# Kernel tuning notes

Hardware: AMD Instinct MI355X
Metric: run time of the kernel (lower is better)

## Reference

```python
import jax, jax.numpy as jnp
import numpy as np

E, C, D, F = 8, 2048, 2048, 8192  # experts, capacity/expert, d_model, d_ff


def setup_inputs() -> dict:
    key = jax.random.key(0)
    k_in, k_w1, k_w2 = jax.random.split(key, 3)
    inputs = jax.random.normal(k_in, (1, E * C, D), dtype=jnp.float32)
    w1 = jax.random.normal(k_w1, (E, D, F), dtype=jnp.float32) * (D ** -0.5)
    b1 = jnp.zeros((E, F), dtype=jnp.float32)
    w2 = jax.random.normal(k_w2, (E, F, D), dtype=jnp.float32) * (F ** -0.5)
    b2 = jnp.zeros((E, D), dtype=jnp.float32)
    return {"inputs": inputs, "w1": w1, "b1": b1, "w2": w2, "b2": b2}


def reference(inputs, w1, b1, w2, b2):
    # inputs: [B, E*C, D]; chunk(dim=1) into E equal chunks == reshape to [B, E, C, D]
    e = w1.shape[0]
    b_, t, d = inputs.shape
    x = inputs.reshape(b_, e, t // e, d)                       # [B,E,C,D]
    # Per-expert FFN: Linear(D->F) + GELU + Linear(F->D), batched over experts
    h = jax.nn.gelu(jnp.einsum("becd,edf->becf", x, w1) + b1[None, :, None, :])
    out = jnp.einsum("becf,efd->becd", h, w2) + b2[None, :, None, :]
    # concat over experts on dim=1 == reshape back to [B, E*C, D]
    return out.reshape(b_, t, d)
```

## Files before the change

### kernel.cpp

```cpp
#include <hip/hip_runtime.h>
#include <hip/hip_bf16.h>
#include <stdint.h>

#define E_ 8
#define C_ 2048
#define D_ 2048
#define F_ 8192

typedef __bf16 bf16x8 __attribute__((ext_vector_type(8)));
typedef float floatx4 __attribute__((ext_vector_type(4)));
typedef uint32_t uint32x4 __attribute__((ext_vector_type(4)));

__device__ __forceinline__ uint16_t f2bf_rne(float f) {
    uint32_t u = __builtin_bit_cast(uint32_t, f);
    u += 0x7fffu + ((u >> 16) & 1u);
    return (uint16_t)(u >> 16);
}

__device__ __forceinline__ float gelu_tanh(float x) {
    float z = 0.7978845608028654f * x * (1.0f + 0.044715f * x * x);
    float e = __expf(2.0f * z);
    float t = 1.0f - 2.0f / (e + 1.0f);
    return 0.5f * x * (1.0f + t);
}

__global__ __launch_bounds__(256) void convert_x_kernel(const float* __restrict__ in,
                                                        uint16_t* __restrict__ out, int n8) {
    int i = blockIdx.x * 256 + threadIdx.x;
    if (i >= n8) return;
    const floatx4* pin = (const floatx4*)in;
    floatx4 a = pin[2 * i];
    floatx4 b = pin[2 * i + 1];
    uint32x4 w;
    w[0] = (uint32_t)f2bf_rne(a[0]) | ((uint32_t)f2bf_rne(a[1]) << 16);
    w[1] = (uint32_t)f2bf_rne(a[2]) | ((uint32_t)f2bf_rne(a[3]) << 16);
    w[2] = (uint32_t)f2bf_rne(b[0]) | ((uint32_t)f2bf_rne(b[1]) << 16);
    w[3] = (uint32_t)f2bf_rne(b[2]) | ((uint32_t)f2bf_rne(b[3]) << 16);
    ((uint32x4*)out)[i] = w;
}

__global__ __launch_bounds__(256) void transpose_convert_kernel(
    const float* __restrict__ in, uint16_t* __restrict__ out,
    int K, int N, int tiles_k, int tiles_n) {
    __shared__ float lds[64 * 65];
    int tiles = tiles_k * tiles_n;
    int e = blockIdx.x / tiles;
    int t = blockIdx.x % tiles;
    int tk = t % tiles_k;
    int tn = t / tiles_k;
    size_t ebase = (size_t)e * K * N;
    int k0 = tk * 64, n0 = tn * 64;
    const float* ip = in + ebase + (size_t)k0 * N + n0;
    int tid = threadIdx.x;
#pragma unroll
    for (int i = 0; i < 4; i++) {
        int lin = i * 256 + tid;
        int r = lin >> 4, c = lin & 15;
        floatx4 v = *(const floatx4*)(ip + (size_t)r * N + c * 4);
        float* l = &lds[r * 65 + c * 4];
        l[0] = v[0]; l[1] = v[1]; l[2] = v[2]; l[3] = v[3];
    }
    __syncthreads();
    uint16_t* op = out + ebase + (size_t)n0 * K + k0;
#pragma unroll
    for (int i = 0; i < 2; i++) {
        int lin = i * 256 + tid;
        int n = lin >> 3, c = lin & 7;
        uint32x4 w;
#pragma unroll
        for (int j = 0; j < 4; j++) {
            float f0 = lds[(c * 8 + 2 * j) * 65 + n];
            float f1 = lds[(c * 8 + 2 * j + 1) * 65 + n];
            w[j] = (uint32_t)f2bf_rne(f0) | ((uint32_t)f2bf_rne(f1) << 16);
        }
        *(uint32x4*)(op + (size_t)n * K + c * 8) = w;
    }
}

template <int GELU>
__global__ __launch_bounds__(256) void gemm_bt_kernel(
    const uint16_t* __restrict__ A,
    const uint16_t* __restrict__ Bt,
    const float* __restrict__ bias,
    void* __restrict__ Out,
    int M, int N, int K, int tiles_m, int tiles_n) {
    __shared__ uint16_t As[128 * 64];
    __shared__ uint16_t Bs[128 * 64];
    int tiles = tiles_m * tiles_n;
    int e = blockIdx.x / tiles;
    int t = blockIdx.x % tiles;
    int bm = t % tiles_m;
    int bn = t / tiles_m;
    int tid = threadIdx.x;
    int lane = tid & 63;
    int wid = tid >> 6;
    int wm = wid >> 1, wn = wid & 1;

    const uint16_t* Ae = A + (size_t)e * M * K;
    const uint16_t* Be = Bt + (size_t)e * N * K;

    int srow = lane >> 3;
    int skk = (lane & 7) * 8;
    const uint16_t* ag[4];
    const uint16_t* bg[4];
#pragma unroll
    for (int j = 0; j < 4; j++) {
        int ch = wid * 4 + j;
        ag[j] = Ae + (size_t)(bm * 128 + ch * 8 + srow) * K + skk;
        bg[j] = Be + (size_t)(bn * 128 + ch * 8 + srow) * K + skk;
    }

    floatx4 acc[4][4];
#pragma unroll
    for (int i = 0; i < 4; i++)
#pragma unroll
        for (int j = 0; j < 4; j++)
#pragma unroll
            for (int r = 0; r < 4; r++) acc[i][j][r] = 0.0f;

    int aoff[4], boff[4];
#pragma unroll
    for (int i = 0; i < 4; i++) {
        aoff[i] = (wm * 64 + i * 16 + (lane & 15)) * 64 + (lane >> 4) * 8;
        boff[i] = (wn * 64 + i * 16 + (lane & 15)) * 64 + (lane >> 4) * 8;
    }

    int kt = K >> 6;
    for (int k0 = 0; k0 < kt; k0++) {
#pragma unroll
        for (int j = 0; j < 4; j++) {
            __builtin_amdgcn_global_load_lds(
                (const __attribute__((address_space(1))) uint32_t*)ag[j],
                (__attribute__((address_space(3))) uint32_t*)&As[(wid * 4 + j) * 512], 16, 0, 0);
            __builtin_amdgcn_global_load_lds(
                (const __attribute__((address_space(1))) uint32_t*)bg[j],
                (__attribute__((address_space(3))) uint32_t*)&Bs[(wid * 4 + j) * 512], 16, 0, 0);
            ag[j] += 64;
            bg[j] += 64;
        }
        __syncthreads();
#pragma unroll
        for (int ks = 0; ks < 2; ks++) {
            bf16x8 fa[4], fb[4];
#pragma unroll
            for (int i = 0; i < 4; i++) {
                fa[i] = *(const bf16x8*)&As[aoff[i] + ks * 32];
                fb[i] = *(const bf16x8*)&Bs[boff[i] + ks * 32];
            }
#pragma unroll
            for (int i = 0; i < 4; i++)
#pragma unroll
                for (int j = 0; j < 4; j++)
                    acc[i][j] = __builtin_amdgcn_mfma_f32_16x16x32_bf16(fa[i], fb[j], acc[i][j], 0, 0, 0);
        }
        __syncthreads();
    }

    int col0 = bn * 128 + wn * 64 + (lane & 15);
    int row0 = bm * 128 + wm * 64 + (lane >> 4) * 4;
    const float* be = bias + (size_t)e * N;
    if (GELU) {
        uint16_t* O = (uint16_t*)Out + (size_t)e * M * N;
#pragma unroll
        for (int j = 0; j < 4; j++) {
            int col = col0 + j * 16;
            float bv = be[col];
#pragma unroll
            for (int i = 0; i < 4; i++) {
                int row = row0 + i * 16;
#pragma unroll
                for (int r = 0; r < 4; r++) {
                    float v = acc[i][j][r] + bv;
                    O[(size_t)(row + r) * N + col] = f2bf_rne(gelu_tanh(v));
                }
            }
        }
    } else {
        float* O = (float*)Out + (size_t)e * M * N;
#pragma unroll
        for (int j = 0; j < 4; j++) {
            int col = col0 + j * 16;
            float bv = be[col];
#pragma unroll
            for (int i = 0; i < 4; i++) {
                int row = row0 + i * 16;
#pragma unroll
                for (int r = 0; r < 4; r++) {
                    O[(size_t)(row + r) * N + col] = acc[i][j][r] + bv;
                }
            }
        }
    }
}

extern "C" void kernel_launch(void* const* d_in, const int* in_sizes, int n_in,
                              void* d_out, int out_size, void* d_ws, size_t ws_size,
                              hipStream_t stream) {
    (void)in_sizes; (void)n_in; (void)out_size; (void)ws_size;
    const float* x  = (const float*)d_in[0];
    const float* w1 = (const float*)d_in[1];
    const float* b1 = (const float*)d_in[2];
    const float* w2 = (const float*)d_in[3];
    const float* b2 = (const float*)d_in[4];
    float* out = (float*)d_out;

    uint16_t* Xb = (uint16_t*)d_ws;
    uint16_t* Wt = Xb + (size_t)E_ * C_ * D_;
    uint16_t* Hb = Wt + (size_t)E_ * D_ * F_;

    int n8 = (E_ * C_ * D_) / 8;
    convert_x_kernel<<<n8 / 256, 256, 0, stream>>>(x, Xb, n8);

    transpose_convert_kernel<<<E_ * (D_ / 64) * (F_ / 64), 256, 0, stream>>>(
        w1, Wt, D_, F_, D_ / 64, F_ / 64);

    gemm_bt_kernel<1><<<E_ * (C_ / 128) * (F_ / 128), 256, 0, stream>>>(
        Xb, Wt, b1, Hb, C_, F_, D_, C_ / 128, F_ / 128);

    transpose_convert_kernel<<<E_ * (F_ / 64) * (D_ / 64), 256, 0, stream>>>(
        w2, Wt, F_, D_, F_ / 64, D_ / 64);

    gemm_bt_kernel<0><<<E_ * (C_ / 128) * (D_ / 128), 256, 0, stream>>>(
        Hb, Wt, b2, out, C_, D_, F_, C_ / 128, D_ / 128);
}
```

Baseline: 2.929 ms.

## Triple-buffer GEMM K-loop with async global-to-LDS prefetch two stages ahead

Restructures the bf16 GEMM main loop into a three-buffer LDS pipeline with a K-step of 32. Loads for step k+2 are issued before the MFMAs of step k, and each step uses a single barrier with explicit vmcnt/lgkmcnt waits. This hides global-memory latency behind compute and removes one barrier per iteration. It also sets launch bounds for 3 blocks per CU and raises wave priority around the MFMA block. The trade-off is more LDS per block, smaller K-steps (more barriers per unit of work) and hand-written wait counts that must match the number of outstanding loads exactly.

```diff
diff --git a/kernel.cpp b/kernel.cpp
--- a/kernel.cpp
+++ b/kernel.cpp
@@ -77,15 +77,20 @@
     }
 }
 
+#define GLL16(gp, lp)                                                    \
+    __builtin_amdgcn_global_load_lds(                                    \
+        (const __attribute__((address_space(1))) uint32_t*)(gp),         \
+        (__attribute__((address_space(3))) uint32_t*)(lp), 16, 0, 0)
+
 template <int GELU>
-__global__ __launch_bounds__(256) void gemm_bt_kernel(
+__global__ __launch_bounds__(256, 3) void gemm_bt_kernel(
     const uint16_t* __restrict__ A,
     const uint16_t* __restrict__ Bt,
     const float* __restrict__ bias,
     void* __restrict__ Out,
     int M, int N, int K, int tiles_m, int tiles_n) {
-    __shared__ uint16_t As[128 * 64];
-    __shared__ uint16_t Bs[128 * 64];
+    __shared__ __align__(16) uint16_t lds[3][8192];
+
     int tiles = tiles_m * tiles_n;
     int e = blockIdx.x / tiles;
     int t = blockIdx.x % tiles;
@@ -99,15 +104,18 @@
     const uint16_t* Ae = A + (size_t)e * M * K;
     const uint16_t* Be = Bt + (size_t)e * N * K;
 
-    int srow = lane >> 3;
-    int skk = (lane & 7) * 8;
-    const uint16_t* ag[4];
-    const uint16_t* bg[4];
-#pragma unroll
-    for (int j = 0; j < 4; j++) {
-        int ch = wid * 4 + j;
-        ag[j] = Ae + (size_t)(bm * 128 + ch * 8 + srow) * K + skk;
-        bg[j] = Be + (size_t)(bn * 128 + ch * 8 + srow) * K + skk;
+    int srow = wid * 16 + (lane >> 2);
+    int scol = (lane & 3) * 8;
+    const uint16_t* Ag = Ae + (size_t)(bm * 128 + srow) * K + scol;
+    const uint16_t* Bg = Be + (size_t)(bn * 128 + srow) * K + scol;
+    int ldsA = wid * 512;
+
+    int l15 = lane & 15, l4 = lane >> 4;
+    int arow[4], brow[4];
+#pragma unroll
+    for (int i = 0; i < 4; i++) {
+        arow[i] = (wm * 64 + i * 16 + l15) * 64 + l4 * 16;
+        brow[i] = 8192 + (wn * 64 + i * 16 + l15) * 64 + l4 * 16;
     }
 
     floatx4 acc[4][4];
@@ -118,42 +126,55 @@
 #pragma unroll
             for (int r = 0; r < 4; r++) acc[i][j][r] = 0.0f;
 
-    int aoff[4], boff[4];
-#pragma unroll
-    for (int i = 0; i < 4; i++) {
-        aoff[i] = (wm * 64 + i * 16 + (lane & 15)) * 64 + (lane >> 4) * 8;
-        boff[i] = (wn * 64 + i * 16 + (lane & 15)) * 64 + (lane >> 4) * 8;
-    }
-
-    int kt = K >> 6;
-    for (int k0 = 0; k0 < kt; k0++) {
-#pragma unroll
-        for (int j = 0; j < 4; j++) {
-            __builtin_amdgcn_global_load_lds(
-                (const __attribute__((address_space(1))) uint32_t*)ag[j],
-                (__attribute__((address_space(3))) uint32_t*)&As[(wid * 4 + j) * 512], 16, 0, 0);
-            __builtin_amdgcn_global_load_lds(
-                (const __attribute__((address_space(1))) uint32_t*)bg[j],
-                (__attribute__((address_space(3))) uint32_t*)&Bs[(wid * 4 + j) * 512], 16, 0, 0);
-            ag[j] += 64;
-            bg[j] += 64;
-        }
-        __syncthreads();
-#pragma unroll
-        for (int ks = 0; ks < 2; ks++) {
-            bf16x8 fa[4], fb[4];
-#pragma unroll
-            for (int i = 0; i < 4; i++) {
-                fa[i] = *(const bf16x8*)&As[aoff[i] + ks * 32];
-                fb[i] = *(const bf16x8*)&Bs[boff[i] + ks * 32];
-            }
-#pragma unroll
-            for (int i = 0; i < 4; i++)
-#pragma unroll
-                for (int j = 0; j < 4; j++)
-                    acc[i][j] = __builtin_amdgcn_mfma_f32_16x16x32_bf16(fa[i], fb[j], acc[i][j], 0, 0, 0);
-        }
-        __syncthreads();
+    int NT = K >> 5;
+
+    auto stage = [&](int buf, int s) {
+        uint16_t* base = &lds[buf][0];
+        size_t k0 = (size_t)s << 5;
+        GLL16(Ag + k0,                  base + ldsA);
+        GLL16(Ag + (size_t)64 * K + k0, base + 2048 + ldsA);
+        GLL16(Bg + k0,                  base + 4096 + ldsA);
+        GLL16(Bg + (size_t)64 * K + k0, base + 6144 + ldsA);
+    };
+
+    stage(0, 0);
+    stage(1, 1);
+    asm volatile("s_waitcnt vmcnt(4)" ::: "memory");
+    __builtin_amdgcn_s_barrier();
+
+    int cb = 0;
+    for (int kt = 0; kt < NT; ++kt) {
+        const char* bufp = (const char*)&lds[cb][0];
+        bf16x8 fa[4], fb[4];
+#pragma unroll
+        for (int i = 0; i < 4; i++) fa[i] = *(const bf16x8*)(bufp + arow[i]);
+#pragma unroll
+        for (int j = 0; j < 4; j++) fb[j] = *(const bf16x8*)(bufp + brow[j]);
+
+        if (kt + 2 < NT) {
+            int pb = cb + 2; if (pb >= 3) pb -= 3;
+            stage(pb, kt + 2);
+        }
+
+        asm volatile("s_waitcnt lgkmcnt(0)" ::: "memory");
+        __builtin_amdgcn_sched_barrier(0);
+
+        __builtin_amdgcn_s_setprio(1);
+#pragma unroll
+        for (int i = 0; i < 4; i++)
+#pragma unroll
+            for (int j = 0; j < 4; j++)
+                acc[i][j] = __builtin_amdgcn_mfma_f32_16x16x32_bf16(fa[i], fb[j], acc[i][j], 0, 0, 0);
+        __builtin_amdgcn_s_setprio(0);
+
+        if (kt < NT - 2) {
+            asm volatile("s_waitcnt vmcnt(4)" ::: "memory");
+            __builtin_amdgcn_s_barrier();
+        } else if (kt == NT - 2) {
+            asm volatile("s_waitcnt vmcnt(0)" ::: "memory");
+            __builtin_amdgcn_s_barrier();
+        }
+        cb++; if (cb == 3) cb = 0;
     }
 
     int col0 = bn * 128 + wn * 64 + (lane & 15);
```

Result: faster. 2.537 ms (-13.4%).
